# Optimization experiments

Measured on AMD Instinct MI355X. Metric: run time of the kernel, lower is better.

Reference implementation:

```python
import jax, jax.numpy as jnp
import numpy as np

B, N, F, L = 8, 2048, 128, 2
SLOPE = 0.1  # LeakyReLU negative slope

def lrelu(v):
    return jnp.where(v >= 0, v, SLOPE * v)

def setup_inputs() -> dict:
    key = jax.random.key(0)
    ks = jax.random.split(key, 7)
    scale = 1.0 / np.sqrt(F)
    return {
        "x": jax.random.normal(ks[0], (B, N, F), dtype=jnp.float32),
        "W3": jax.random.normal(ks[1], (L, F, F), dtype=jnp.float32) * scale,
        "b3": jnp.zeros((L, F), dtype=jnp.float32),
        "W4": jax.random.normal(ks[2], (L, F, F), dtype=jnp.float32) * scale,
        "b4": jnp.zeros((L, F), dtype=jnp.float32),
        "W5": jax.random.normal(ks[3], (L, F, F), dtype=jnp.float32) * scale,
        "b5": jnp.zeros((L, F), dtype=jnp.float32),
    }

def reference(x, W3, b3, W4, b4, W5, b5):
    # GraphStack of L GraphLayer modules, mes_type '0':
    #   weight_ij = dot(LeakyReLU(g3(n_i)), LeakyReLU(g4(n_j)))
    #   message_i = mean_{j != i} weight_ij * n_j
    #   n_i_out   = LeakyReLU(g5(message_i)) + n_i
    n = x.shape[1]
    for l in range(W3.shape[0]):
        w1 = lrelu(jnp.einsum('bnf,fg->bng', x, W3[l]) + b3[l])  # [B,N,F]
        w2 = lrelu(jnp.einsum('bnf,fg->bng', x, W4[l]) + b4[l])  # [B,N,F]
        wt = jnp.einsum('bif,bjf->bij', w1, w2)                  # pairwise weights [B,N,N]
        diag = jnp.einsum('bif,bif->bi', w1, w2)                 # self weights to exclude
        msg = (jnp.einsum('bij,bjf->bif', wt, x) - diag[..., None] * x) / (n - 1)
        x = lrelu(jnp.einsum('bif,fg->big', msg, W5[l]) + b5[l]) + x
    return x
```

## Files before the change

### kernel.cpp

```cpp
#include <hip/hip_runtime.h>

#define BB 8
#define NN 2048
#define FF 128
#define NL 2
#define SLOPE 0.1f
#define NROW (BB * NN)
#define XS_STRIDE 136

typedef __attribute__((ext_vector_type(8))) short short8;
typedef __attribute__((ext_vector_type(4))) float f32x4;

__device__ __forceinline__ float lrelu(float v) { return v >= 0.f ? v : SLOPE * v; }

__device__ __forceinline__ ushort f2bf(float f) {
    uint u = __float_as_uint(f);
    return (ushort)((u + 0x7fffu + ((u >> 16) & 1u)) >> 16);
}

__global__ __launch_bounds__(256) void k_prep(
    const float* __restrict__ W3, const float* __restrict__ W4,
    const float* __restrict__ W5, ushort* __restrict__ Wt)
{
    const int idx = blockIdx.x * 256 + threadIdx.x;
    const int m = idx >> 14;
    const int rem = idx & 16383;
    const int f = rem & 127;
    const int g = rem >> 7;
    const int l = m / 3, w = m % 3;
    const float* src = (w == 0) ? W3 : (w == 1) ? W4 : W5;
    Wt[m * 16384 + g * 128 + f] = f2bf(src[l * 16384 + f * 128 + g]);
}

__global__ __launch_bounds__(256) void k_w12(
    const float* __restrict__ x, const ushort* __restrict__ w3t,
    const ushort* __restrict__ w4t, const float* __restrict__ b3,
    const float* __restrict__ b4, ushort* __restrict__ w1b,
    ushort* __restrict__ w2t, ushort* __restrict__ xt,
    float* __restrict__ diag)
{
    __shared__ ushort xs[32 * XS_STRIDE];
    __shared__ float diag_s[32];

    const int tid = threadIdx.x;
    const int row0 = blockIdx.x * 32;
    const int b = row0 >> 11;
    const int jloc0 = row0 & 2047;

    if (tid < 32) diag_s[tid] = 0.f;

    const float4* xg4 = (const float4*)(x + (size_t)row0 * FF);
#pragma unroll
    for (int i = 0; i < 4; i++) {
        const int f4 = i * 256 + tid;
        const int row = f4 >> 5;
        const int k = (f4 & 31) * 4;
        float4 v = xg4[f4];
        ushort4 h;
        h.x = f2bf(v.x); h.y = f2bf(v.y); h.z = f2bf(v.z); h.w = f2bf(v.w);
        *(ushort4*)&xs[row * XS_STRIDE + k] = h;
    }
    __syncthreads();

    {
        const int g = tid >> 1;
        const int h = tid & 1;
        uint p[8];
#pragma unroll
        for (int jj = 0; jj < 8; jj++) {
            const uint lo = xs[(h * 16 + jj * 2) * XS_STRIDE + g];
            const uint hi = xs[(h * 16 + jj * 2 + 1) * XS_STRIDE + g];
            p[jj] = lo | (hi << 16);
        }
        uint4* dst = (uint4*)&xt[(size_t)b * (FF * NN) + (size_t)g * NN + jloc0 + h * 16];
        dst[0] = make_uint4(p[0], p[1], p[2], p[3]);
        dst[1] = make_uint4(p[4], p[5], p[6], p[7]);
    }

    const int lane = tid & 63;
    const int wave = tid >> 6;
    const int c = lane & 15;
    const int quad = lane >> 4;
    const int ct0 = wave * 2;

    f32x4 acc1[2][2], acc2[2][2];
#pragma unroll
    for (int rt = 0; rt < 2; rt++)
#pragma unroll
        for (int ct = 0; ct < 2; ct++) { acc1[rt][ct] = (f32x4)0.f; acc2[rt][ct] = (f32x4)0.f; }

#pragma unroll
    for (int kk = 0; kk < 4; kk++) {
        short8 a0 = *(const short8*)&xs[c * XS_STRIDE + kk * 32 + quad * 8];
        short8 a1 = *(const short8*)&xs[(16 + c) * XS_STRIDE + kk * 32 + quad * 8];
#pragma unroll
        for (int ct = 0; ct < 2; ct++) {
            const int n = (ct0 + ct) * 16 + c;
            short8 bf3 = *(const short8*)&w3t[n * 128 + kk * 32 + quad * 8];
            short8 bf4 = *(const short8*)&w4t[n * 128 + kk * 32 + quad * 8];
            acc1[0][ct] = __builtin_amdgcn_mfma_f32_16x16x32_bf16(a0, bf3, acc1[0][ct], 0, 0, 0);
            acc1[1][ct] = __builtin_amdgcn_mfma_f32_16x16x32_bf16(a1, bf3, acc1[1][ct], 0, 0, 0);
            acc2[0][ct] = __builtin_amdgcn_mfma_f32_16x16x32_bf16(a0, bf4, acc2[0][ct], 0, 0, 0);
            acc2[1][ct] = __builtin_amdgcn_mfma_f32_16x16x32_bf16(a1, bf4, acc2[1][ct], 0, 0, 0);
        }
    }

    float dpar[2][4];
#pragma unroll
    for (int rt = 0; rt < 2; rt++)
#pragma unroll
        for (int r = 0; r < 4; r++) dpar[rt][r] = 0.f;

#pragma unroll
    for (int rt = 0; rt < 2; rt++) {
#pragma unroll
        for (int ct = 0; ct < 2; ct++) {
            const int gcol = (ct0 + ct) * 16 + c;
            const float bb3 = b3[gcol], bb4 = b4[gcol];
            ushort w2p[4];
#pragma unroll
            for (int r = 0; r < 4; r++) {
                const float v1 = lrelu(acc1[rt][ct][r] + bb3);
                const float v2 = lrelu(acc2[rt][ct][r] + bb4);
                const int grow = row0 + rt * 16 + quad * 4 + r;
                w1b[(size_t)grow * FF + gcol] = f2bf(v1);
                w2p[r] = f2bf(v2);
                dpar[rt][r] += v1 * v2;
            }
            const uint lo = (uint)w2p[0] | ((uint)w2p[1] << 16);
            const uint hi = (uint)w2p[2] | ((uint)w2p[3] << 16);
            uint2* dst = (uint2*)&w2t[(size_t)b * (FF * NN) + (size_t)gcol * NN +
                                      jloc0 + rt * 16 + quad * 4];
            *dst = make_uint2(lo, hi);
        }
    }

#pragma unroll
    for (int rt = 0; rt < 2; rt++) {
#pragma unroll
        for (int r = 0; r < 4; r++) {
            float dp = dpar[rt][r];
            dp += __shfl_xor(dp, 1, 64);
            dp += __shfl_xor(dp, 2, 64);
            dp += __shfl_xor(dp, 4, 64);
            dp += __shfl_xor(dp, 8, 64);
            if (c == 0) atomicAdd(&diag_s[rt * 16 + quad * 4 + r], dp);
        }
    }
    __syncthreads();
    if (tid < 32) diag[row0 + tid] = diag_s[tid];
}

__global__ __launch_bounds__(256) void k_S2(
    const ushort* __restrict__ xt, const ushort* __restrict__ w2t,
    ushort* __restrict__ St)
{
    __shared__ float red[4][512];
    const int tid = threadIdx.x;
    const int lane = tid & 63;
    const int wave = tid >> 6;
    const int c = lane & 15;
    const int quad = lane >> 4;

    const int b  = blockIdx.x >> 5;
    const int gq = (blockIdx.x >> 3) & 3;
    const int fs = blockIdx.x & 7;

    const ushort* xtb = xt + (size_t)b * (FF * NN);
    const ushort* w2b = w2t + (size_t)b * (FF * NN);

    const int j0 = wave * 512 + quad * 8;
    const ushort* a0p = &xtb[(gq * 32 + c) * NN + j0];
    const ushort* a1p = &xtb[(gq * 32 + 16 + c) * NN + j0];
    const ushort* bp  = &w2b[(fs * 16 + c) * NN + j0];

    f32x4 acc0 = (f32x4)0.f, acc1 = (f32x4)0.f;
#pragma unroll
    for (int it = 0; it < 16; it++) {
        short8 a0 = *(const short8*)(a0p + it * 32);
        short8 a1 = *(const short8*)(a1p + it * 32);
        short8 bf = *(const short8*)(bp + it * 32);
        acc0 = __builtin_amdgcn_mfma_f32_16x16x32_bf16(a0, bf, acc0, 0, 0, 0);
        acc1 = __builtin_amdgcn_mfma_f32_16x16x32_bf16(a1, bf, acc1, 0, 0, 0);
    }

#pragma unroll
    for (int r = 0; r < 4; r++) {
        red[wave][(quad * 4 + r) * 16 + c] = acc0[r];
        red[wave][(16 + quad * 4 + r) * 16 + c] = acc1[r];
    }
    __syncthreads();

#pragma unroll
    for (int i = 0; i < 2; i++) {
        const int idx = i * 256 + tid;
        const float s = red[0][idx] + red[1][idx] + red[2][idx] + red[3][idx];
        const int gl = idx >> 4;
        const int fl = idx & 15;
        St[(size_t)b * (FF * FF) + (size_t)(gq * 32 + gl) * FF + fs * 16 + fl] = f2bf(s);
    }
}

__global__ __launch_bounds__(256) void k_out(
    const float* __restrict__ x, const ushort* __restrict__ w1b,
    const ushort* __restrict__ St, const float* __restrict__ diag,
    const ushort* __restrict__ w5t, const float* __restrict__ b5,
    float* __restrict__ out)
{
    __shared__ ushort w1s[32 * XS_STRIDE];
    __shared__ ushort ms[32 * XS_STRIDE];

    const int tid = threadIdx.x;
    const int row0 = blockIdx.x * 32;
    const int b = row0 >> 11;
    const ushort* Sb = St + (size_t)b * (FF * FF);

#pragma unroll
    for (int i = 0; i < 2; i++) {
        const int e8 = i * 256 + tid;
        const int off = e8 * 8;
        const int row = off >> 7;
        const int k = off & 127;
        short8 v = *(const short8*)&w1b[(size_t)row0 * FF + off];
        *(short8*)&w1s[row * XS_STRIDE + k] = v;
    }
    __syncthreads();

    const int lane = tid & 63;
    const int wave = tid >> 6;
    const int c = lane & 15;
    const int quad = lane >> 4;
    const int ct0 = wave * 2;

    f32x4 accm[2][2];
#pragma unroll
    for (int rt = 0; rt < 2; rt++)
#pragma unroll
        for (int ct = 0; ct < 2; ct++) accm[rt][ct] = (f32x4)0.f;

#pragma unroll
    for (int kk = 0; kk < 4; kk++) {
        short8 a0 = *(const short8*)&w1s[c * XS_STRIDE + kk * 32 + quad * 8];
        short8 a1 = *(const short8*)&w1s[(16 + c) * XS_STRIDE + kk * 32 + quad * 8];
#pragma unroll
        for (int ct = 0; ct < 2; ct++) {
            const int n = (ct0 + ct) * 16 + c;
            short8 bf = *(const short8*)&Sb[n * 128 + kk * 32 + quad * 8];
            accm[0][ct] = __builtin_amdgcn_mfma_f32_16x16x32_bf16(a0, bf, accm[0][ct], 0, 0, 0);
            accm[1][ct] = __builtin_amdgcn_mfma_f32_16x16x32_bf16(a1, bf, accm[1][ct], 0, 0, 0);
        }
    }

    const float inv = 1.f / (float)(NN - 1);
    float xsv[2][2][4];
#pragma unroll
    for (int rt = 0; rt < 2; rt++) {
        float dg[4];
#pragma unroll
        for (int r = 0; r < 4; r++) dg[r] = diag[row0 + rt * 16 + quad * 4 + r];
#pragma unroll
        for (int ct = 0; ct < 2; ct++) {
            const int gcol = (ct0 + ct) * 16 + c;
#pragma unroll
            for (int r = 0; r < 4; r++) {
                const int lrow = rt * 16 + quad * 4 + r;
                const float xv = x[(size_t)(row0 + lrow) * FF + gcol];
                xsv[rt][ct][r] = xv;
                const float m = (accm[rt][ct][r] - dg[r] * xv) * inv;
                ms[lrow * XS_STRIDE + gcol] = f2bf(m);
            }
        }
    }
    __syncthreads();

    f32x4 acc2[2][2];
#pragma unroll
    for (int rt = 0; rt < 2; rt++)
#pragma unroll
        for (int ct = 0; ct < 2; ct++) acc2[rt][ct] = (f32x4)0.f;

#pragma unroll
    for (int kk = 0; kk < 4; kk++) {
        short8 a0 = *(const short8*)&ms[c * XS_STRIDE + kk * 32 + quad * 8];
        short8 a1 = *(const short8*)&ms[(16 + c) * XS_STRIDE + kk * 32 + quad * 8];
#pragma unroll
        for (int ct = 0; ct < 2; ct++) {
            const int n = (ct0 + ct) * 16 + c;
            short8 bf = *(const short8*)&w5t[n * 128 + kk * 32 + quad * 8];
            acc2[0][ct] = __builtin_amdgcn_mfma_f32_16x16x32_bf16(a0, bf, acc2[0][ct], 0, 0, 0);
            acc2[1][ct] = __builtin_amdgcn_mfma_f32_16x16x32_bf16(a1, bf, acc2[1][ct], 0, 0, 0);
        }
    }

#pragma unroll
    for (int rt = 0; rt < 2; rt++) {
#pragma unroll
        for (int ct = 0; ct < 2; ct++) {
            const int gcol = (ct0 + ct) * 16 + c;
            const float bb = b5[gcol];
#pragma unroll
            for (int r = 0; r < 4; r++) {
                const int grow = row0 + rt * 16 + quad * 4 + r;
                out[(size_t)grow * FF + gcol] = lrelu(acc2[rt][ct][r] + bb) + xsv[rt][ct][r];
            }
        }
    }
}

__global__ __launch_bounds__(256) void k_out_w12(
    const float* __restrict__ x, const ushort* __restrict__ w1b_in,
    const ushort* __restrict__ St, const float* __restrict__ diag_in,
    const ushort* __restrict__ w5t, const float* __restrict__ b5,
    float* __restrict__ out,
    const ushort* __restrict__ w3t, const ushort* __restrict__ w4t,
    const float* __restrict__ b3, const float* __restrict__ b4,
    ushort* __restrict__ w1b, ushort* __restrict__ w2t,
    ushort* __restrict__ xt, float* __restrict__ diag)
{
    __shared__ ushort sA[32 * XS_STRIDE];
    __shared__ ushort sB[32 * XS_STRIDE];
    __shared__ float diag_s[32];

    const int tid = threadIdx.x;
    const int row0 = blockIdx.x * 32;
    const int b = row0 >> 11;
    const int jloc0 = row0 & 2047;
    const ushort* Sb = St + (size_t)b * (FF * FF);

    if (tid < 32) diag_s[tid] = 0.f;

#pragma unroll
    for (int i = 0; i < 2; i++) {
        const int e8 = i * 256 + tid;
        const int off = e8 * 8;
        const int row = off >> 7;
        const int k = off & 127;
        short8 v = *(const short8*)&w1b_in[(size_t)row0 * FF + off];
        *(short8*)&sA[row * XS_STRIDE + k] = v;
    }
    __syncthreads();

    const int lane = tid & 63;
    const int wave = tid >> 6;
    const int c = lane & 15;
    const int quad = lane >> 4;
    const int ct0 = wave * 2;

    f32x4 accm[2][2];
#pragma unroll
    for (int rt = 0; rt < 2; rt++)
#pragma unroll
        for (int ct = 0; ct < 2; ct++) accm[rt][ct] = (f32x4)0.f;

#pragma unroll
    for (int kk = 0; kk < 4; kk++) {
        short8 a0 = *(const short8*)&sA[c * XS_STRIDE + kk * 32 + quad * 8];
        short8 a1 = *(const short8*)&sA[(16 + c) * XS_STRIDE + kk * 32 + quad * 8];
#pragma unroll
        for (int ct = 0; ct < 2; ct++) {
            const int n = (ct0 + ct) * 16 + c;
            short8 bf = *(const short8*)&Sb[n * 128 + kk * 32 + quad * 8];
            accm[0][ct] = __builtin_amdgcn_mfma_f32_16x16x32_bf16(a0, bf, accm[0][ct], 0, 0, 0);
            accm[1][ct] = __builtin_amdgcn_mfma_f32_16x16x32_bf16(a1, bf, accm[1][ct], 0, 0, 0);
        }
    }

    const float inv = 1.f / (float)(NN - 1);
    float xsv[2][2][4];
#pragma unroll
    for (int rt = 0; rt < 2; rt++) {
        float dg[4];
#pragma unroll
        for (int r = 0; r < 4; r++) dg[r] = diag_in[row0 + rt * 16 + quad * 4 + r];
#pragma unroll
        for (int ct = 0; ct < 2; ct++) {
            const int gcol = (ct0 + ct) * 16 + c;
#pragma unroll
            for (int r = 0; r < 4; r++) {
                const int lrow = rt * 16 + quad * 4 + r;
                const float xv = x[(size_t)(row0 + lrow) * FF + gcol];
                xsv[rt][ct][r] = xv;
                const float m = (accm[rt][ct][r] - dg[r] * xv) * inv;
                sB[lrow * XS_STRIDE + gcol] = f2bf(m);
            }
        }
    }
    __syncthreads();

    f32x4 acc2[2][2];
#pragma unroll
    for (int rt = 0; rt < 2; rt++)
#pragma unroll
        for (int ct = 0; ct < 2; ct++) acc2[rt][ct] = (f32x4)0.f;

#pragma unroll
    for (int kk = 0; kk < 4; kk++) {
        short8 a0 = *(const short8*)&sB[c * XS_STRIDE + kk * 32 + quad * 8];
        short8 a1 = *(const short8*)&sB[(16 + c) * XS_STRIDE + kk * 32 + quad * 8];
#pragma unroll
        for (int ct = 0; ct < 2; ct++) {
            const int n = (ct0 + ct) * 16 + c;
            short8 bf = *(const short8*)&w5t[n * 128 + kk * 32 + quad * 8];
            acc2[0][ct] = __builtin_amdgcn_mfma_f32_16x16x32_bf16(a0, bf, acc2[0][ct], 0, 0, 0);
            acc2[1][ct] = __builtin_amdgcn_mfma_f32_16x16x32_bf16(a1, bf, acc2[1][ct], 0, 0, 0);
        }
    }

#pragma unroll
    for (int rt = 0; rt < 2; rt++) {
#pragma unroll
        for (int ct = 0; ct < 2; ct++) {
            const int gcol = (ct0 + ct) * 16 + c;
            const float bb = b5[gcol];
#pragma unroll
            for (int r = 0; r < 4; r++) {
                const int lrow = rt * 16 + quad * 4 + r;
                const float ov = lrelu(acc2[rt][ct][r] + bb) + xsv[rt][ct][r];
                out[(size_t)(row0 + lrow) * FF + gcol] = ov;
                sA[lrow * XS_STRIDE + gcol] = f2bf(ov);
            }
        }
    }
    __syncthreads();

    {
        const int g = tid >> 1;
        const int h = tid & 1;
        uint p[8];
#pragma unroll
        for (int jj = 0; jj < 8; jj++) {
            const uint lo = sA[(h * 16 + jj * 2) * XS_STRIDE + g];
            const uint hi = sA[(h * 16 + jj * 2 + 1) * XS_STRIDE + g];
            p[jj] = lo | (hi << 16);
        }
        uint4* dst = (uint4*)&xt[(size_t)b * (FF * NN) + (size_t)g * NN + jloc0 + h * 16];
        dst[0] = make_uint4(p[0], p[1], p[2], p[3]);
        dst[1] = make_uint4(p[4], p[5], p[6], p[7]);
    }

    f32x4 acc1n[2][2], acc2n[2][2];
#pragma unroll
    for (int rt = 0; rt < 2; rt++)
#pragma unroll
        for (int ct = 0; ct < 2; ct++) { acc1n[rt][ct] = (f32x4)0.f; acc2n[rt][ct] = (f32x4)0.f; }

#pragma unroll
    for (int kk = 0; kk < 4; kk++) {
        short8 a0 = *(const short8*)&sA[c * XS_STRIDE + kk * 32 + quad * 8];
        short8 a1 = *(const short8*)&sA[(16 + c) * XS_STRIDE + kk * 32 + quad * 8];
#pragma unroll
        for (int ct = 0; ct < 2; ct++) {
            const int n = (ct0 + ct) * 16 + c;
            short8 bf3 = *(const short8*)&w3t[n * 128 + kk * 32 + quad * 8];
            short8 bf4 = *(const short8*)&w4t[n * 128 + kk * 32 + quad * 8];
            acc1n[0][ct] = __builtin_amdgcn_mfma_f32_16x16x32_bf16(a0, bf3, acc1n[0][ct], 0, 0, 0);
            acc1n[1][ct] = __builtin_amdgcn_mfma_f32_16x16x32_bf16(a1, bf3, acc1n[1][ct], 0, 0, 0);
            acc2n[0][ct] = __builtin_amdgcn_mfma_f32_16x16x32_bf16(a0, bf4, acc2n[0][ct], 0, 0, 0);
            acc2n[1][ct] = __builtin_amdgcn_mfma_f32_16x16x32_bf16(a1, bf4, acc2n[1][ct], 0, 0, 0);
        }
    }

    float dpar[2][4];
#pragma unroll
    for (int rt = 0; rt < 2; rt++)
#pragma unroll
        for (int r = 0; r < 4; r++) dpar[rt][r] = 0.f;

#pragma unroll
    for (int rt = 0; rt < 2; rt++) {
#pragma unroll
        for (int ct = 0; ct < 2; ct++) {
            const int gcol = (ct0 + ct) * 16 + c;
            const float bb3 = b3[gcol], bb4 = b4[gcol];
            ushort w2p[4];
#pragma unroll
            for (int r = 0; r < 4; r++) {
                const float v1 = lrelu(acc1n[rt][ct][r] + bb3);
                const float v2 = lrelu(acc2n[rt][ct][r] + bb4);
                const int grow = row0 + rt * 16 + quad * 4 + r;
                w1b[(size_t)grow * FF + gcol] = f2bf(v1);
                w2p[r] = f2bf(v2);
                dpar[rt][r] += v1 * v2;
            }
            const uint lo = (uint)w2p[0] | ((uint)w2p[1] << 16);
            const uint hi = (uint)w2p[2] | ((uint)w2p[3] << 16);
            uint2* dst = (uint2*)&w2t[(size_t)b * (FF * NN) + (size_t)gcol * NN +
                                      jloc0 + rt * 16 + quad * 4];
            *dst = make_uint2(lo, hi);
        }
    }

#pragma unroll
    for (int rt = 0; rt < 2; rt++) {
#pragma unroll
        for (int r = 0; r < 4; r++) {
            float dp = dpar[rt][r];
            dp += __shfl_xor(dp, 1, 64);
            dp += __shfl_xor(dp, 2, 64);
            dp += __shfl_xor(dp, 4, 64);
            dp += __shfl_xor(dp, 8, 64);
            if (c == 0) atomicAdd(&diag_s[rt * 16 + quad * 4 + r], dp);
        }
    }
    __syncthreads();
    if (tid < 32) diag[row0 + tid] = diag_s[tid];
}

extern "C" void kernel_launch(void* const* d_in, const int* in_sizes, int n_in,
                              void* d_out, int out_size, void* d_ws, size_t ws_size,
                              hipStream_t stream)
{
    const float* x  = (const float*)d_in[0];
    const float* W3 = (const float*)d_in[1];
    const float* b3 = (const float*)d_in[2];
    const float* W4 = (const float*)d_in[3];
    const float* b4 = (const float*)d_in[4];
    const float* W5 = (const float*)d_in[5];
    const float* b5 = (const float*)d_in[6];
    float* out = (float*)d_out;

    char* ws = (char*)d_ws;
    ushort* w1b   = (ushort*)(ws);
    ushort* w2t   = (ushort*)(ws + ((size_t)4  << 20));
    ushort* xt    = (ushort*)(ws + ((size_t)8  << 20));
    float*  diag  = (float*) (ws + ((size_t)12 << 20));
    ushort* St    = (ushort*)(ws + ((size_t)13 << 20));
    ushort* Wt    = (ushort*)(ws + ((size_t)14 << 20));

    const ushort* w3t0 = Wt;
    const ushort* w4t0 = Wt + 16384;
    const ushort* w5t0 = Wt + 2 * 16384;
    const ushort* w3t1 = Wt + 3 * 16384;
    const ushort* w4t1 = Wt + 4 * 16384;
    const ushort* w5t1 = Wt + 5 * 16384;

    const int rowBlocks = NROW / 32;

    k_prep<<<384, 256, 0, stream>>>(W3, W4, W5, Wt);

    k_w12<<<rowBlocks, 256, 0, stream>>>(x, w3t0, w4t0, b3, b4, w1b, w2t, xt, diag);
    k_S2<<<256, 256, 0, stream>>>(xt, w2t, St);
    k_out_w12<<<rowBlocks, 256, 0, stream>>>(x, w1b, St, diag, w5t0, b5, out,
                                             w3t1, w4t1, b3 + FF, b4 + FF,
                                             w1b, w2t, xt, diag);
    k_S2<<<256, 256, 0, stream>>>(xt, w2t, St);
    k_out<<<rowBlocks, 256, 0, stream>>>(out, w1b, St, diag, w5t1, b5 + FF, out);
}
```

Baseline: 122.5 us.

## Use 64-row, 512-thread blocks with one column tile per wave in row kernels

```diff
diff --git a/kernel.cpp b/kernel.cpp
--- a/kernel.cpp
+++ b/kernel.cpp
@@ -32,27 +32,27 @@
     Wt[m * 16384 + g * 128 + f] = f2bf(src[l * 16384 + f * 128 + g]);
 }
 
-__global__ __launch_bounds__(256) void k_w12(
+__global__ __launch_bounds__(512) void k_w12(
     const float* __restrict__ x, const ushort* __restrict__ w3t,
     const ushort* __restrict__ w4t, const float* __restrict__ b3,
     const float* __restrict__ b4, ushort* __restrict__ w1b,
     ushort* __restrict__ w2t, ushort* __restrict__ xt,
     float* __restrict__ diag)
 {
-    __shared__ ushort xs[32 * XS_STRIDE];
-    __shared__ float diag_s[32];
+    __shared__ ushort xs[64 * XS_STRIDE];
+    __shared__ float diag_s[64];
 
     const int tid = threadIdx.x;
-    const int row0 = blockIdx.x * 32;
+    const int row0 = blockIdx.x * 64;
     const int b = row0 >> 11;
     const int jloc0 = row0 & 2047;
 
-    if (tid < 32) diag_s[tid] = 0.f;
+    if (tid < 64) diag_s[tid] = 0.f;
 
     const float4* xg4 = (const float4*)(x + (size_t)row0 * FF);
 #pragma unroll
     for (int i = 0; i < 4; i++) {
-        const int f4 = i * 256 + tid;
+        const int f4 = i * 512 + tid;
         const int row = f4 >> 5;
         const int k = (f4 & 31) * 4;
         float4 v = xg4[f4];
@@ -63,8 +63,8 @@
     __syncthreads();
 
     {
-        const int g = tid >> 1;
-        const int h = tid & 1;
+        const int g = tid >> 2;
+        const int h = tid & 3;
         uint p[8];
 #pragma unroll
         for (int jj = 0; jj < 8; jj++) {
@@ -81,62 +81,49 @@
     const int wave = tid >> 6;
     const int c = lane & 15;
     const int quad = lane >> 4;
-    const int ct0 = wave * 2;
-
-    f32x4 acc1[2][2], acc2[2][2];
-#pragma unroll
-    for (int rt = 0; rt < 2; rt++)
-#pragma unroll
-        for (int ct = 0; ct < 2; ct++) { acc1[rt][ct] = (f32x4)0.f; acc2[rt][ct] = (f32x4)0.f; }
-
-#pragma unroll
-    for (int kk = 0; kk < 4; kk++) {
-        short8 a0 = *(const short8*)&xs[c * XS_STRIDE + kk * 32 + quad * 8];
-        short8 a1 = *(const short8*)&xs[(16 + c) * XS_STRIDE + kk * 32 + quad * 8];
-#pragma unroll
-        for (int ct = 0; ct < 2; ct++) {
-            const int n = (ct0 + ct) * 16 + c;
-            short8 bf3 = *(const short8*)&w3t[n * 128 + kk * 32 + quad * 8];
-            short8 bf4 = *(const short8*)&w4t[n * 128 + kk * 32 + quad * 8];
-            acc1[0][ct] = __builtin_amdgcn_mfma_f32_16x16x32_bf16(a0, bf3, acc1[0][ct], 0, 0, 0);
-            acc1[1][ct] = __builtin_amdgcn_mfma_f32_16x16x32_bf16(a1, bf3, acc1[1][ct], 0, 0, 0);
-            acc2[0][ct] = __builtin_amdgcn_mfma_f32_16x16x32_bf16(a0, bf4, acc2[0][ct], 0, 0, 0);
-            acc2[1][ct] = __builtin_amdgcn_mfma_f32_16x16x32_bf16(a1, bf4, acc2[1][ct], 0, 0, 0);
-        }
-    }
-
-    float dpar[2][4];
-#pragma unroll
-    for (int rt = 0; rt < 2; rt++)
-#pragma unroll
-        for (int r = 0; r < 4; r++) dpar[rt][r] = 0.f;
-
-#pragma unroll
-    for (int rt = 0; rt < 2; rt++) {
-#pragma unroll
-        for (int ct = 0; ct < 2; ct++) {
-            const int gcol = (ct0 + ct) * 16 + c;
-            const float bb3 = b3[gcol], bb4 = b4[gcol];
-            ushort w2p[4];
-#pragma unroll
-            for (int r = 0; r < 4; r++) {
-                const float v1 = lrelu(acc1[rt][ct][r] + bb3);
-                const float v2 = lrelu(acc2[rt][ct][r] + bb4);
-                const int grow = row0 + rt * 16 + quad * 4 + r;
-                w1b[(size_t)grow * FF + gcol] = f2bf(v1);
-                w2p[r] = f2bf(v2);
-                dpar[rt][r] += v1 * v2;
-            }
-            const uint lo = (uint)w2p[0] | ((uint)w2p[1] << 16);
-            const uint hi = (uint)w2p[2] | ((uint)w2p[3] << 16);
-            uint2* dst = (uint2*)&w2t[(size_t)b * (FF * NN) + (size_t)gcol * NN +
-                                      jloc0 + rt * 16 + quad * 4];
-            *dst = make_uint2(lo, hi);
-        }
-    }
-
-#pragma unroll
-    for (int rt = 0; rt < 2; rt++) {
+    const int n = wave * 16 + c;
+
+    f32x4 acc1[4], acc2[4];
+#pragma unroll
+    for (int rt = 0; rt < 4; rt++) { acc1[rt] = (f32x4)0.f; acc2[rt] = (f32x4)0.f; }
+
+#pragma unroll
+    for (int kk = 0; kk < 4; kk++) {
+        short8 bf3 = *(const short8*)&w3t[n * 128 + kk * 32 + quad * 8];
+        short8 bf4 = *(const short8*)&w4t[n * 128 + kk * 32 + quad * 8];
+#pragma unroll
+        for (int rt = 0; rt < 4; rt++) {
+            short8 a = *(const short8*)&xs[(rt * 16 + c) * XS_STRIDE + kk * 32 + quad * 8];
+            acc1[rt] = __builtin_amdgcn_mfma_f32_16x16x32_bf16(a, bf3, acc1[rt], 0, 0, 0);
+            acc2[rt] = __builtin_amdgcn_mfma_f32_16x16x32_bf16(a, bf4, acc2[rt], 0, 0, 0);
+        }
+    }
+
+    const int gcol = wave * 16 + c;
+    const float bb3 = b3[gcol], bb4 = b4[gcol];
+    float dpar[4][4];
+
+#pragma unroll
+    for (int rt = 0; rt < 4; rt++) {
+        ushort w2p[4];
+#pragma unroll
+        for (int r = 0; r < 4; r++) {
+            const float v1 = lrelu(acc1[rt][r] + bb3);
+            const float v2 = lrelu(acc2[rt][r] + bb4);
+            const int grow = row0 + rt * 16 + quad * 4 + r;
+            w1b[(size_t)grow * FF + gcol] = f2bf(v1);
+            w2p[r] = f2bf(v2);
+            dpar[rt][r] = v1 * v2;
+        }
+        const uint lo = (uint)w2p[0] | ((uint)w2p[1] << 16);
+        const uint hi = (uint)w2p[2] | ((uint)w2p[3] << 16);
+        uint2* dst = (uint2*)&w2t[(size_t)b * (FF * NN) + (size_t)gcol * NN +
+                                  jloc0 + rt * 16 + quad * 4];
+        *dst = make_uint2(lo, hi);
+    }
+
+#pragma unroll
+    for (int rt = 0; rt < 4; rt++) {
 #pragma unroll
         for (int r = 0; r < 4; r++) {
             float dp = dpar[rt][r];
@@ -148,7 +135,7 @@
         }
     }
     __syncthreads();
-    if (tid < 32) diag[row0 + tid] = diag_s[tid];
+    if (tid < 64) diag[row0 + tid] = diag_s[tid];
 }
 
 __global__ __launch_bounds__(256) void k_S2(
@@ -201,24 +188,23 @@
     }
 }
 
-__global__ __launch_bounds__(256) void k_out(
+__global__ __launch_bounds__(512) void k_out(
     const float* __restrict__ x, const ushort* __restrict__ w1b,
     const ushort* __restrict__ St, const float* __restrict__ diag,
     const ushort* __restrict__ w5t, const float* __restrict__ b5,
     float* __restrict__ out)
 {
-    __shared__ ushort w1s[32 * XS_STRIDE];
-    __shared__ ushort ms[32 * XS_STRIDE];
+    __shared__ ushort w1s[64 * XS_STRIDE];
+    __shared__ ushort ms[64 * XS_STRIDE];
 
     const int tid = threadIdx.x;
-    const int row0 = blockIdx.x * 32;
+    const int row0 = blockIdx.x * 64;
     const int b = row0 >> 11;
     const ushort* Sb = St + (size_t)b * (FF * FF);
 
 #pragma unroll
     for (int i = 0; i < 2; i++) {
-        const int e8 = i * 256 + tid;
-        const int off = e8 * 8;
+        const int off = (i * 512 + tid) * 8;
         const int row = off >> 7;
         const int k = off & 127;
         short8 v = *(const short8*)&w1b[(size_t)row0 * FF + off];
@@ -230,84 +216,67 @@
     const int wave = tid >> 6;
     const int c = lane & 15;
     const int quad = lane >> 4;
-    const int ct0 = wave * 2;
-
-    f32x4 accm[2][2];
-#pragma unroll
-    for (int rt = 0; rt < 2; rt++)
-#pragma unroll
-        for (int ct = 0; ct < 2; ct++) accm[rt][ct] = (f32x4)0.f;
-
-#pragma unroll
-    for (int kk = 0; kk < 4; kk++) {
-        short8 a0 = *(const short8*)&w1s[c * XS_STRIDE + kk * 32 + quad * 8];
-        short8 a1 = *(const short8*)&w1s[(16 + c) * XS_STRIDE + kk * 32 + quad * 8];
-#pragma unroll
-        for (int ct = 0; ct < 2; ct++) {
-            const int n = (ct0 + ct) * 16 + c;
-            short8 bf = *(const short8*)&Sb[n * 128 + kk * 32 + quad * 8];
-            accm[0][ct] = __builtin_amdgcn_mfma_f32_16x16x32_bf16(a0, bf, accm[0][ct], 0, 0, 0);
-            accm[1][ct] = __builtin_amdgcn_mfma_f32_16x16x32_bf16(a1, bf, accm[1][ct], 0, 0, 0);
+    const int n = wave * 16 + c;
+
+    f32x4 accm[4];
+#pragma unroll
+    for (int rt = 0; rt < 4; rt++) accm[rt] = (f32x4)0.f;
+
+#pragma unroll
+    for (int kk = 0; kk < 4; kk++) {
+        short8 bf = *(const short8*)&Sb[n * 128 + kk * 32 + quad * 8];
+#pragma unroll
+        for (int rt = 0; rt < 4; rt++) {
+            short8 a = *(const short8*)&w1s[(rt * 16 + c) * XS_STRIDE + kk * 32 + quad * 8];
+            accm[rt] = __builtin_amdgcn_mfma_f32_16x16x32_bf16(a, bf, accm[rt], 0, 0, 0);
         }
     }
 
     const float inv = 1.f / (float)(NN - 1);
-    float xsv[2][2][4];
-#pragma unroll
-    for (int rt = 0; rt < 2; rt++) {
+    const int gcol = wave * 16 + c;
+    float xsv[4][4];
+#pragma unroll
+    for (int rt = 0; rt < 4; rt++) {
         float dg[4];
 #pragma unroll
         for (int r = 0; r < 4; r++) dg[r] = diag[row0 + rt * 16 + quad * 4 + r];
 #pragma unroll
-        for (int ct = 0; ct < 2; ct++) {
-            const int gcol = (ct0 + ct) * 16 + c;
-#pragma unroll
-            for (int r = 0; r < 4; r++) {
-                const int lrow = rt * 16 + quad * 4 + r;
-                const float xv = x[(size_t)(row0 + lrow) * FF + gcol];
-                xsv[rt][ct][r] = xv;
-                const float m = (accm[rt][ct][r] - dg[r] * xv) * inv;
-                ms[lrow * XS_STRIDE + gcol] = f2bf(m);
-            }
-        }
-    }
-    __syncthreads();
-
-    f32x4 acc2[2][2];
-#pragma unroll
-    for (int rt = 0; rt < 2; rt++)
-#pragma unroll
-        for (int ct = 0; ct < 2; ct++) acc2[rt][ct] = (f32x4)0.f;
-
-#pragma unroll
-    for (int kk = 0; kk < 4; kk++) {
-        short8 a0 = *(const short8*)&ms[c * XS_STRIDE + kk * 32 + quad * 8];
-        short8 a1 = *(const short8*)&ms[(16 + c) * XS_STRIDE + kk * 32 + quad * 8];
-#pragma unroll
-        for (int ct = 0; ct < 2; ct++) {
-            const int n = (ct0 + ct) * 16 + c;
-            short8 bf = *(const short8*)&w5t[n * 128 + kk * 32 + quad * 8];
-            acc2[0][ct] = __builtin_amdgcn_mfma_f32_16x16x32_bf16(a0, bf, acc2[0][ct], 0, 0, 0);
-            acc2[1][ct] = __builtin_amdgcn_mfma_f32_16x16x32_bf16(a1, bf, acc2[1][ct], 0, 0, 0);
-        }
-    }
-
-#pragma unroll
-    for (int rt = 0; rt < 2; rt++) {
-#pragma unroll
-        for (int ct = 0; ct < 2; ct++) {
-            const int gcol = (ct0 + ct) * 16 + c;
-            const float bb = b5[gcol];
-#pragma unroll
-            for (int r = 0; r < 4; r++) {
-                const int grow = row0 + rt * 16 + quad * 4 + r;
-                out[(size_t)grow * FF + gcol] = lrelu(acc2[rt][ct][r] + bb) + xsv[rt][ct][r];
-            }
-        }
-    }
-}
-
-__global__ __launch_bounds__(256) void k_out_w12(
+        for (int r = 0; r < 4; r++) {
+            const int lrow = rt * 16 + quad * 4 + r;
+            const float xv = x[(size_t)(row0 + lrow) * FF + gcol];
+            xsv[rt][r] = xv;
+            const float m = (accm[rt][r] - dg[r] * xv) * inv;
+            ms[lrow * XS_STRIDE + gcol] = f2bf(m);
+        }
+    }
+    __syncthreads();
+
+    f32x4 acc2[4];
+#pragma unroll
+    for (int rt = 0; rt < 4; rt++) acc2[rt] = (f32x4)0.f;
+
+#pragma unroll
+    for (int kk = 0; kk < 4; kk++) {
+        short8 bf = *(const short8*)&w5t[n * 128 + kk * 32 + quad * 8];
+#pragma unroll
+        for (int rt = 0; rt < 4; rt++) {
+            short8 a = *(const short8*)&ms[(rt * 16 + c) * XS_STRIDE + kk * 32 + quad * 8];
+            acc2[rt] = __builtin_amdgcn_mfma_f32_16x16x32_bf16(a, bf, acc2[rt], 0, 0, 0);
+        }
+    }
+
+    const float bb = b5[gcol];
+#pragma unroll
+    for (int rt = 0; rt < 4; rt++) {
+#pragma unroll
+        for (int r = 0; r < 4; r++) {
+            const int grow = row0 + rt * 16 + quad * 4 + r;
+            out[(size_t)grow * FF + gcol] = lrelu(acc2[rt][r] + bb) + xsv[rt][r];
+        }
+    }
+}
+
+__global__ __launch_bounds__(512) void k_out_w12(
     const float* __restrict__ x, const ushort* __restrict__ w1b_in,
     const ushort* __restrict__ St, const float* __restrict__ diag_in,
     const ushort* __restrict__ w5t, const float* __restrict__ b5,
@@ -317,22 +286,21 @@
     ushort* __restrict__ w1b, ushort* __restrict__ w2t,
     ushort* __restrict__ xt, float* __restrict__ diag)
 {
-    __shared__ ushort sA[32 * XS_STRIDE];
-    __shared__ ushort sB[32 * XS_STRIDE];
-    __shared__ float diag_s[32];
+    __shared__ ushort sA[64 * XS_STRIDE];
+    __shared__ ushort sB[64 * XS_STRIDE];
+    __shared__ float diag_s[64];
 
     const int tid = threadIdx.x;
-    const int row0 = blockIdx.x * 32;
+    const int row0 = blockIdx.x * 64;
     const int b = row0 >> 11;
     const int jloc0 = row0 & 2047;
     const ushort* Sb = St + (size_t)b * (FF * FF);
 
-    if (tid < 32) diag_s[tid] = 0.f;
+    if (tid < 64) diag_s[tid] = 0.f;
 
 #pragma unroll
     for (int i = 0; i < 2; i++) {
-        const int e8 = i * 256 + tid;
-        const int off = e8 * 8;
+        const int off = (i * 512 + tid) * 8;
         const int row = off >> 7;
         const int k = off & 127;
         short8 v = *(const short8*)&w1b_in[(size_t)row0 * FF + off];
@@ -344,88 +312,71 @@
     const int wave = tid >> 6;
     const int c = lane & 15;
     const int quad = lane >> 4;
-    const int ct0 = wave * 2;
-
-    f32x4 accm[2][2];
-#pragma unroll
-    for (int rt = 0; rt < 2; rt++)
-#pragma unroll
-        for (int ct = 0; ct < 2; ct++) accm[rt][ct] = (f32x4)0.f;
-
-#pragma unroll
-    for (int kk = 0; kk < 4; kk++) {
-        short8 a0 = *(const short8*)&sA[c * XS_STRIDE + kk * 32 + quad * 8];
-        short8 a1 = *(const short8*)&sA[(16 + c) * XS_STRIDE + kk * 32 + quad * 8];
-#pragma unroll
-        for (int ct = 0; ct < 2; ct++) {
-            const int n = (ct0 + ct) * 16 + c;
-            short8 bf = *(const short8*)&Sb[n * 128 + kk * 32 + quad * 8];
-            accm[0][ct] = __builtin_amdgcn_mfma_f32_16x16x32_bf16(a0, bf, accm[0][ct], 0, 0, 0);
-            accm[1][ct] = __builtin_amdgcn_mfma_f32_16x16x32_bf16(a1, bf, accm[1][ct], 0, 0, 0);
+    const int n = wave * 16 + c;
+    const int gcol = wave * 16 + c;
+
+    f32x4 accm[4];
+#pragma unroll
+    for (int rt = 0; rt < 4; rt++) accm[rt] = (f32x4)0.f;
+
+#pragma unroll
+    for (int kk = 0; kk < 4; kk++) {
+        short8 bf = *(const short8*)&Sb[n * 128 + kk * 32 + quad * 8];
+#pragma unroll
+        for (int rt = 0; rt < 4; rt++) {
+            short8 a = *(const short8*)&sA[(rt * 16 + c) * XS_STRIDE + kk * 32 + quad * 8];
+            accm[rt] = __builtin_amdgcn_mfma_f32_16x16x32_bf16(a, bf, accm[rt], 0, 0, 0);
         }
     }
 
     const float inv = 1.f / (float)(NN - 1);
-    float xsv[2][2][4];
-#pragma unroll
-    for (int rt = 0; rt < 2; rt++) {
+    float xsv[4][4];
+#pragma unroll
+    for (int rt = 0; rt < 4; rt++) {
         float dg[4];
 #pragma unroll
         for (int r = 0; r < 4; r++) dg[r] = diag_in[row0 + rt * 16 + quad * 4 + r];
 #pragma unroll
-        for (int ct = 0; ct < 2; ct++) {
-            const int gcol = (ct0 + ct) * 16 + c;
-#pragma unroll
-            for (int r = 0; r < 4; r++) {
-                const int lrow = rt * 16 + quad * 4 + r;
-                const float xv = x[(size_t)(row0 + lrow) * FF + gcol];
-                xsv[rt][ct][r] = xv;
-                const float m = (accm[rt][ct][r] - dg[r] * xv) * inv;
-                sB[lrow * XS_STRIDE + gcol] = f2bf(m);
-            }
-        }
-    }
-    __syncthreads();
-
-    f32x4 acc2[2][2];
-#pragma unroll
-    for (int rt = 0; rt < 2; rt++)
-#pragma unroll
-        for (int ct = 0; ct < 2; ct++) acc2[rt][ct] = (f32x4)0.f;
-
-#pragma unroll
-    for (int kk = 0; kk < 4; kk++) {
-        short8 a0 = *(const short8*)&sB[c * XS_STRIDE + kk * 32 + quad * 8];
-        short8 a1 = *(const short8*)&sB[(16 + c) * XS_STRIDE + kk * 32 + quad * 8];
-#pragma unroll
-        for (int ct = 0; ct < 2; ct++) {
-            const int n = (ct0 + ct) * 16 + c;
-            short8 bf = *(const short8*)&w5t[n * 128 + kk * 32 + quad * 8];
-            acc2[0][ct] = __builtin_amdgcn_mfma_f32_16x16x32_bf16(a0, bf, acc2[0][ct], 0, 0, 0);
-            acc2[1][ct] = __builtin_amdgcn_mfma_f32_16x16x32_bf16(a1, bf, acc2[1][ct], 0, 0, 0);
-        }
-    }
-
-#pragma unroll
-    for (int rt = 0; rt < 2; rt++) {
-#pragma unroll
-        for (int ct = 0; ct < 2; ct++) {
-            const int gcol = (ct0 + ct) * 16 + c;
-            const float bb = b5[gcol];
-#pragma unroll
-            for (int r = 0; r < 4; r++) {
-                const int lrow = rt * 16 + quad * 4 + r;
-                const float ov = lrelu(acc2[rt][ct][r] + bb) + xsv[rt][ct][r];
-                out[(size_t)(row0 + lrow) * FF + gcol] = ov;
-                sA[lrow * XS_STRIDE + gcol] = f2bf(ov);
-            }
+        for (int r = 0; r < 4; r++) {
+            const int lrow = rt * 16 + quad * 4 + r;
+            const float xv = x[(size_t)(row0 + lrow) * FF + gcol];
+            xsv[rt][r] = xv;
+            const float m = (accm[rt][r] - dg[r] * xv) * inv;
+            sB[lrow * XS_STRIDE + gcol] = f2bf(m);
+        }
+    }
+    __syncthreads();
+
+    f32x4 acc2[4];
+#pragma unroll
+    for (int rt = 0; rt < 4; rt++) acc2[rt] = (f32x4)0.f;
+
+#pragma unroll
+    for (int kk = 0; kk < 4; kk++) {
+        short8 bf = *(const short8*)&w5t[n * 128 + kk * 32 + quad * 8];
+#pragma unroll
+        for (int rt = 0; rt < 4; rt++) {
+            short8 a = *(const short8*)&sB[(rt * 16 + c) * XS_STRIDE + kk * 32 + quad * 8];
+            acc2[rt] = __builtin_amdgcn_mfma_f32_16x16x32_bf16(a, bf, acc2[rt], 0, 0, 0);
+        }
+    }
+
+    const float bb = b5[gcol];
+#pragma unroll
+    for (int rt = 0; rt < 4; rt++) {
+#pragma unroll
+        for (int r = 0; r < 4; r++) {
+            const int lrow = rt * 16 + quad * 4 + r;
+            const float ov = lrelu(acc2[rt][r] + bb) + xsv[rt][r];
+            out[(size_t)(row0 + lrow) * FF + gcol] = ov;
+            sA[lrow * XS_STRIDE + gcol] = f2bf(ov);
         }
     }
     __syncthreads();
 
     {
-        const int g = tid >> 1;
-        const int h = tid & 1;
+        const int g = tid >> 2;
+        const int h = tid & 3;
         uint p[8];
 #pragma unroll
         for (int jj = 0; jj < 8; jj++) {
@@ -438,60 +389,45 @@
         dst[1] = make_uint4(p[4], p[5], p[6], p[7]);
     }
 
-    f32x4 acc1n[2][2], acc2n[2][2];
-#pragma unroll
-    for (int rt = 0; rt < 2; rt++)
-#pragma unroll
-        for (int ct = 0; ct < 2; ct++) { acc1n[rt][ct] = (f32x4)0.f; acc2n[rt][ct] = (f32x4)0.f; }
-
-#pragma unroll
-    for (int kk = 0; kk < 4; kk++) {
-        short8 a0 = *(const short8*)&sA[c * XS_STRIDE + kk * 32 + quad * 8];
-        short8 a1 = *(const short8*)&sA[(16 + c) * XS_STRIDE + kk * 32 + quad * 8];
-#pragma unroll
-        for (int ct = 0; ct < 2; ct++) {
-            const int n = (ct0 + ct) * 16 + c;
-            short8 bf3 = *(const short8*)&w3t[n * 128 + kk * 32 + quad * 8];
-            short8 bf4 = *(const short8*)&w4t[n * 128 + kk * 32 + quad * 8];
-            acc1n[0][ct] = __builtin_amdgcn_mfma_f32_16x16x32_bf16(a0, bf3, acc1n[0][ct], 0, 0, 0);
-            acc1n[1][ct] = __builtin_amdgcn_mfma_f32_16x16x32_bf16(a1, bf3, acc1n[1][ct], 0, 0, 0);
-            acc2n[0][ct] = __builtin_amdgcn_mfma_f32_16x16x32_bf16(a0, bf4, acc2n[0][ct], 0, 0, 0);
-            acc2n[1][ct] = __builtin_amdgcn_mfma_f32_16x16x32_bf16(a1, bf4, acc2n[1][ct], 0, 0, 0);
-        }
-    }
-
-    float dpar[2][4];
-#pragma unroll
-    for (int rt = 0; rt < 2; rt++)
-#pragma unroll
-        for (int r = 0; r < 4; r++) dpar[rt][r] = 0.f;
-
-#pragma unroll
-    for (int rt = 0; rt < 2; rt++) {
-#pragma unroll
-        for (int ct = 0; ct < 2; ct++) {
-            const int gcol = (ct0 + ct) * 16 + c;
-            const float bb3 = b3[gcol], bb4 = b4[gcol];
-            ushort w2p[4];
-#pragma unroll
-            for (int r = 0; r < 4; r++) {
-                const float v1 = lrelu(acc1n[rt][ct][r] + bb3);
-                const float v2 = lrelu(acc2n[rt][ct][r] + bb4);
-                const int grow = row0 + rt * 16 + quad * 4 + r;
-                w1b[(size_t)grow * FF + gcol] = f2bf(v1);
-                w2p[r] = f2bf(v2);
-                dpar[rt][r] += v1 * v2;
-            }
-            const uint lo = (uint)w2p[0] | ((uint)w2p[1] << 16);
-            const uint hi = (uint)w2p[2] | ((uint)w2p[3] << 16);
-            uint2* dst = (uint2*)&w2t[(size_t)b * (FF * NN) + (size_t)gcol * NN +
-                                      jloc0 + rt * 16 + quad * 4];
-            *dst = make_uint2(lo, hi);
-        }
-    }
-
-#pragma unroll
-    for (int rt = 0; rt < 2; rt++) {
+    f32x4 acc1n[4], acc2n[4];
+#pragma unroll
+    for (int rt = 0; rt < 4; rt++) { acc1n[rt] = (f32x4)0.f; acc2n[rt] = (f32x4)0.f; }
+
+#pragma unroll
+    for (int kk = 0; kk < 4; kk++) {
+        short8 bf3 = *(const short8*)&w3t[n * 128 + kk * 32 + quad * 8];
+        short8 bf4 = *(const short8*)&w4t[n * 128 + kk * 32 + quad * 8];
+#pragma unroll
+        for (int rt = 0; rt < 4; rt++) {
+            short8 a = *(const short8*)&sA[(rt * 16 + c) * XS_STRIDE + kk * 32 + quad * 8];
+            acc1n[rt] = __builtin_amdgcn_mfma_f32_16x16x32_bf16(a, bf3, acc1n[rt], 0, 0, 0);
+            acc2n[rt] = __builtin_amdgcn_mfma_f32_16x16x32_bf16(a, bf4, acc2n[rt], 0, 0, 0);
+        }
+    }
+
+    const float bb3 = b3[gcol], bb4 = b4[gcol];
+    float dpar[4][4];
+#pragma unroll
+    for (int rt = 0; rt < 4; rt++) {
+        ushort w2p[4];
+#pragma unroll
+        for (int r = 0; r < 4; r++) {
+            const float v1 = lrelu(acc1n[rt][r] + bb3);
+            const float v2 = lrelu(acc2n[rt][r] + bb4);
+            const int grow = row0 + rt * 16 + quad * 4 + r;
+            w1b[(size_t)grow * FF + gcol] = f2bf(v1);
+            w2p[r] = f2bf(v2);
+            dpar[rt][r] = v1 * v2;
+        }
+        const uint lo = (uint)w2p[0] | ((uint)w2p[1] << 16);
+        const uint hi = (uint)w2p[2] | ((uint)w2p[3] << 16);
+        uint2* dst = (uint2*)&w2t[(size_t)b * (FF * NN) + (size_t)gcol * NN +
+                                  jloc0 + rt * 16 + quad * 4];
+        *dst = make_uint2(lo, hi);
+    }
+
+#pragma unroll
+    for (int rt = 0; rt < 4; rt++) {
 #pragma unroll
         for (int r = 0; r < 4; r++) {
             float dp = dpar[rt][r];
@@ -503,7 +439,7 @@
         }
     }
     __syncthreads();
-    if (tid < 32) diag[row0 + tid] = diag_s[tid];
+    if (tid < 64) diag[row0 + tid] = diag_s[tid];
 }
 
 extern "C" void kernel_launch(void* const* d_in, const int* in_sizes, int n_in,
@@ -534,15 +470,15 @@
     const ushort* w4t1 = Wt + 4 * 16384;
     const ushort* w5t1 = Wt + 5 * 16384;
 
-    const int rowBlocks = NROW / 32;
+    const int rowBlocks = NROW / 64;
 
     k_prep<<<384, 256, 0, stream>>>(W3, W4, W5, Wt);
 
-    k_w12<<<rowBlocks, 256, 0, stream>>>(x, w3t0, w4t0, b3, b4, w1b, w2t, xt, diag);
+    k_w12<<<rowBlocks, 512, 0, stream>>>(x, w3t0, w4t0, b3, b4, w1b, w2t, xt, diag);
     k_S2<<<256, 256, 0, stream>>>(xt, w2t, St);
-    k_out_w12<<<rowBlocks, 256, 0, stream>>>(x, w1b, St, diag, w5t0, b5, out,
+    k_out_w12<<<rowBlocks, 512, 0, stream>>>(x, w1b, St, diag, w5t0, b5, out,
                                              w3t1, w4t1, b3 + FF, b4 + FF,
                                              w1b, w2t, xt, diag);
     k_S2<<<256, 256, 0, stream>>>(xt, w2t, St);
-    k_out<<<rowBlocks, 256, 0, stream>>>(out, w1b, St, diag, w5t1, b5 + FF, out);
-}
+    k_out<<<rowBlocks, 512, 0, stream>>>(out, w1b, St, diag, w5t1, b5 + FF, out);
+}
```

New measurement: 120.6 us. Within noise of the previous version (-1.6%).
